# Kernel tuning notes

Hardware: AMD Instinct MI355X
Metric: run time of the kernel (lower is better)

Reference implementation:

```python
import jax, jax.numpy as jnp
import numpy as np

N_NODES = 10000


def _sage_pool(h, src, dst, Wp, bp, Ws, Wn, b):
    # DGL SAGEConv 'pool': m = relu(fc_pool(h_src)); neigh = max over in-edges;
    # out = fc_self(h_dst) + fc_neigh(neigh) + bias. Zero-in-degree nodes get 0 neigh.
    m = jax.nn.relu(h @ Wp + bp)                      # [N, d_in] node-level transform
    neigh = jax.ops.segment_max(m[src], dst, num_segments=N_NODES)  # [N, d_in]
    neigh = jnp.where(jnp.isfinite(neigh), neigh, 0.0)  # empty segments filled -inf -> 0
    return h @ Ws + neigh @ Wn + b


def setup_inputs() -> dict:
    key = jax.random.key(0)
    ks = jax.random.split(key, 20)
    dims = [(960, 512), (512, 512), (512, 1)]
    inp = {
        "h": jax.random.normal(ks[0], (N_NODES, 960), dtype=jnp.float32),
        "src": jax.random.randint(ks[1], (160000,), 0, N_NODES),
        "dst": jax.random.randint(ks[2], (160000,), 0, N_NODES),
    }
    ki = 3
    for l, (di, do) in enumerate(dims):
        inp[f"Wp{l}"] = jax.random.normal(ks[ki + 0], (di, di), dtype=jnp.float32) * 0.02
        inp[f"bp{l}"] = jnp.zeros((di,), dtype=jnp.float32)
        inp[f"Ws{l}"] = jax.random.normal(ks[ki + 1], (di, do), dtype=jnp.float32) * 0.02
        inp[f"Wn{l}"] = jax.random.normal(ks[ki + 2], (di, do), dtype=jnp.float32) * 0.02
        inp[f"b{l}"] = jnp.zeros((do,), dtype=jnp.float32)
        ki += 3
    return inp


def reference(h, src, dst,
              Wp0, bp0, Ws0, Wn0, b0,
              Wp1, bp1, Ws1, Wn1, b1,
              Wp2, bp2, Ws2, Wn2, b2):
    # layer 0: 960 -> 512, relu (dropout = identity in eval)
    x = jax.nn.relu(_sage_pool(h, src, dst, Wp0, bp0, Ws0, Wn0, b0))
    # layer 1: 512 -> 512, relu
    x = jax.nn.relu(_sage_pool(x, src, dst, Wp1, bp1, Ws1, Wn1, b1))
    # layer 2: 512 -> 1, sigmoid, squeeze -> per-node prediction
    x = _sage_pool(x, src, dst, Wp2, bp2, Ws2, Wn2, b2)
    return jax.nn.sigmoid(x).squeeze(-1)  # [N]
```

## Files before the change

### kernel.cpp

```cpp
#include <hip/hip_runtime.h>
#include <stdint.h>

#define NN 10000
#define NE 160000
#define MPAD 10112
#define MTILES 79

typedef unsigned short u16;
typedef float f32x4 __attribute__((ext_vector_type(4)));
typedef short short8 __attribute__((ext_vector_type(8)));
typedef __bf16 bf16x8 __attribute__((ext_vector_type(8)));
typedef unsigned short u16x4 __attribute__((ext_vector_type(4)));
typedef unsigned short u16x8 __attribute__((ext_vector_type(8)));

__device__ __forceinline__ float bf2f(u16 u) {
  union { unsigned u; float f; } c; c.u = ((unsigned)u) << 16; return c.f;
}
__device__ __forceinline__ u16 f2bf(float f) {
  union { float f; unsigned u; } c; c.f = f;
  return (u16)((c.u + 0x7FFFu + ((c.u >> 16) & 1u)) >> 16);
}

__device__ __forceinline__ void gld_lds16(void* lds, const void* g) {
  __builtin_amdgcn_global_load_lds(
      (const unsigned int __attribute__((address_space(1)))*)g,
      (unsigned int __attribute__((address_space(3)))*)lds, 16, 0, 0);
}

__global__ __launch_bounds__(256) void deg_count(const int* __restrict__ dst, int* __restrict__ deg) {
  int e = blockIdx.x * 256 + threadIdx.x;
  if (e < NE) atomicAdd(&deg[dst[e]], 1);
}

__global__ __launch_bounds__(256) void scan_off(const int* __restrict__ deg,
                                                int* __restrict__ roff, int* __restrict__ cur) {
  __shared__ int part[256];
  const int t = threadIdx.x;
  const int CH = 40;
  int s = 0;
  for (int i = 0; i < CH; ++i) { int idx = t * CH + i; if (idx < NN) s += deg[idx]; }
  part[t] = s; __syncthreads();
  for (int off = 1; off < 256; off <<= 1) {
    int v = (t >= off) ? part[t - off] : 0;
    __syncthreads(); part[t] += v; __syncthreads();
  }
  int run = (t == 0) ? 0 : part[t - 1];
  for (int i = 0; i < CH; ++i) {
    int idx = t * CH + i;
    if (idx < NN) { roff[idx] = run; cur[idx] = run; run += deg[idx]; }
  }
  if (t == 255) roff[NN] = NE;
}

__global__ __launch_bounds__(256) void fill_csr(const int* __restrict__ src, const int* __restrict__ dst,
                                                int* __restrict__ cur, int* __restrict__ esrc) {
  int e = blockIdx.x * 256 + threadIdx.x;
  if (e < NE) {
    int p = atomicAdd(&cur[dst[e]], 1);
    esrc[p] = src[e];
  }
}

__global__ __launch_bounds__(256) void convert_h(const float* __restrict__ h, u16* __restrict__ hbf) {
  const size_t i = (size_t)(blockIdx.x * 256 + threadIdx.x) * 4;
  if (i >= (size_t)MPAD * 960) return;
  u16x4 o;
  if (i < (size_t)NN * 960) {
    float4 v = *(const float4*)(h + i);
    o[0] = f2bf(v.x); o[1] = f2bf(v.y); o[2] = f2bf(v.z); o[3] = f2bf(v.w);
  } else {
    o[0] = 0; o[1] = 0; o[2] = 0; o[3] = 0;
  }
  *(u16x4*)(hbf + i) = o;
}

struct WDesc { const float* in; u16* out; int R, C, Cpad, ldo, koff; };
struct WPack { WDesc d[7]; };

__global__ __launch_bounds__(256) void transpose_all(WPack p) {
  const WDesc w = p.d[blockIdx.z];
  const int cb = blockIdx.x * 32, rb = blockIdx.y * 32;
  if (cb >= w.Cpad || rb >= w.R) return;
  __shared__ float tile[32][33];
  const int tx = threadIdx.x & 31, ty = threadIdx.x >> 5;
  for (int i = ty; i < 32; i += 8) {
    int r = rb + i, c = cb + tx;
    tile[i][tx] = (r < w.R && c < w.C) ? w.in[(size_t)r * w.C + c] : 0.f;
  }
  __syncthreads();
  for (int i = ty; i < 32; i += 8) {
    int c = cb + i, r = rb + tx;
    if (c < w.Cpad && r < w.R) w.out[(size_t)c * w.ldo + w.koff + r] = f2bf(tile[tx][i]);
  }
}

template<int TM, int TN, int MINW>
__global__ __launch_bounds__(512, MINW) void gemm3(
    const u16* __restrict__ A0, int lda0,
    const u16* __restrict__ A1, int lda1, int ksplit,
    const u16* __restrict__ B,
    const float* __restrict__ bias, int nbias,
    u16* __restrict__ Cb, int ldcb,
    int K, int act, int tiles_n) {
  constexpr int TR = TM + TN;
  constexpr int NC = TR * 128 / (512 * 16);
  constexpr int WCOLS = 4;
  constexpr int WN = TN / WCOLS;
  constexpr int NJ = WN / 16;
  constexpr int MT = MPAD / TM;
  __shared__ __align__(16) u16 S0[TR * 64];
  __shared__ __align__(16) u16 S1[TR * 64];
  const int tid = threadIdx.x;
  const int wave = tid >> 6, lane = tid & 63;

  const int nwg = tiles_n * MT;
  const int orig = blockIdx.x + blockIdx.y * tiles_n;
  const int q = nwg >> 3, r8 = nwg & 7;
  const int xcd = orig & 7, idx = orig >> 3;
  const int wg = (xcd < r8 ? xcd * (q + 1) : r8 * (q + 1) + (xcd - r8) * q) + idx;
  const int tm = (wg / tiles_n) * TM;
  const int tn = (wg % tiles_n) * TN;

  const int wr = (wave / WCOLS) * 64;
  const int wc = (wave % WCOLS) * WN;
  const int fr = lane & 15, fq = lane >> 4;
  const int sr8 = lane >> 3;
  const int sslot = lane & 7;
  f32x4 acc[4][NJ] = {};

  auto stage = [&](u16* Sw, int kk) {
#pragma unroll
    for (int c = 0; c < NC; ++c) {
      const int row = c * 64 + wave * 8 + sr8;
      const int gs = (sslot ^ (row & 7)) * 8;
      const void* g;
      if (c < NC * TM / TR) {
        g = (kk < ksplit)
            ? (const void*)&A0[(size_t)(tm + row) * lda0 + kk + gs]
            : (const void*)&A1[(size_t)(tm + row) * lda1 + (kk - ksplit) + gs];
      } else {
        g = (const void*)&B[(size_t)(tn + row - TM) * (size_t)K + kk + gs];
      }
      gld_lds16(&Sw[(c * 64 + wave * 8) * 64], g);
    }
  };

  const int nsteps = K >> 6;
  stage(S0, 0);
  stage(S1, 64);
  for (int base = 0; base < nsteps; base += 2) {
#pragma unroll
    for (int ph = 0; ph < 2; ++ph) {
      const int t = base + ph;
      if (t >= nsteps) break;
      u16* Sr = (ph == 0) ? S0 : S1;
      if (t + 1 < nsteps) {
        asm volatile("s_waitcnt vmcnt(%0)" :: "i"(NC) : "memory");
      } else {
        asm volatile("s_waitcnt vmcnt(0)" ::: "memory");
      }
      __builtin_amdgcn_s_barrier();
      __builtin_amdgcn_sched_barrier(0);
      short8 af[4][2], bfr[2][NJ];
#pragma unroll
      for (int i = 0; i < 4; ++i) {
        const int r = wr + i * 16 + fr;
#pragma unroll
        for (int kc = 0; kc < 2; ++kc)
          af[i][kc] = *(const short8*)&Sr[r * 64 + ((((kc << 2) | fq) ^ (r & 7)) << 3)];
      }
#pragma unroll
      for (int j = 0; j < NJ; ++j) {
        const int r = TM + wc + j * 16 + fr;
#pragma unroll
        for (int kc = 0; kc < 2; ++kc)
          bfr[kc][j] = *(const short8*)&Sr[r * 64 + ((((kc << 2) | fq) ^ (r & 7)) << 3)];
      }
      asm volatile("s_waitcnt lgkmcnt(0)" ::: "memory");
      __builtin_amdgcn_sched_barrier(0);
      __builtin_amdgcn_s_barrier();
      if (t + 2 < nsteps) stage(Sr, (t + 2) << 6);
      __builtin_amdgcn_s_setprio(1);
#pragma unroll
      for (int kc = 0; kc < 2; ++kc)
#pragma unroll
        for (int i = 0; i < 4; ++i)
#pragma unroll
          for (int j = 0; j < NJ; ++j)
            acc[i][j] = __builtin_amdgcn_mfma_f32_16x16x32_bf16(
                __builtin_bit_cast(bf16x8, af[i][kc]), __builtin_bit_cast(bf16x8, bfr[kc][j]),
                acc[i][j], 0, 0, 0);
      __builtin_amdgcn_s_setprio(0);
      __builtin_amdgcn_sched_barrier(0);
    }
  }

  const int cr = fq * 4, cc = fr;
#pragma unroll
  for (int i = 0; i < 4; ++i)
#pragma unroll
    for (int j = 0; j < NJ; ++j) {
      const int col = tn + wc + j * 16 + cc;
      const float bv = (col < nbias) ? bias[col] : 0.f;
#pragma unroll
      for (int r = 0; r < 4; ++r) {
        const int row = tm + wr + i * 16 + cr + r;
        float v = acc[i][j][r] + bv;
        if (act) v = fmaxf(v, 0.f);
        Cb[(size_t)row * ldcb + col] = f2bf(v);
      }
    }
}

template<int CW>
__global__ __launch_bounds__(256) void aggregate_xcd(
    const u16* __restrict__ m, int ldm, const int* __restrict__ roff,
    const int* __restrict__ esrc, u16* __restrict__ neigh, int ldn) {
  constexpr int TPN = CW / 8;
  constexpr int NPB = 256 / TPN;
  const int chunk = blockIdx.x & 7;
  const int node = (blockIdx.x >> 3) * NPB + threadIdx.x / TPN;
  if (node >= NN) return;
  const int fi = chunk * CW + (threadIdx.x % TPN) * 8;
  const int beg = roff[node], end = roff[node + 1];
  u16x8 a;
#pragma unroll
  for (int i = 0; i < 8; ++i) a[i] = 0;
  for (int e = beg; e < end; ++e) {
    const u16* row = m + (size_t)esrc[e] * ldm;
    u16x8 v = *(const u16x8*)(row + fi);
#pragma unroll
    for (int i = 0; i < 8; ++i) a[i] = (v[i] > a[i]) ? v[i] : a[i];
  }
  *(u16x8*)(neigh + (size_t)node * ldn + fi) = a;
}

__global__ __launch_bounds__(256) void final_out(
    const u16* __restrict__ x, const u16* __restrict__ neigh,
    const float* __restrict__ ws, const float* __restrict__ wn,
    const float* __restrict__ b, float* __restrict__ out) {
  const int wave = threadIdx.x >> 6, lane = threadIdx.x & 63;
  const int n = blockIdx.x * 4 + wave;
  if (n >= NN) return;
  const int f = lane * 8;
  const u16* xr = x + (size_t)n * 512 + f;
  const u16* nr = neigh + (size_t)n * 512 + f;
  float s = 0.f;
#pragma unroll
  for (int i = 0; i < 8; ++i)
    s += bf2f(xr[i]) * ws[f + i] + bf2f(nr[i]) * wn[f + i];
#pragma unroll
  for (int o = 32; o > 0; o >>= 1) s += __shfl_xor(s, o);
  if (lane == 0) out[n] = 1.f / (1.f + expf(-(s + b[0])));
}

extern "C" void kernel_launch(void* const* d_in, const int* in_sizes, int n_in,
                              void* d_out, int out_size, void* d_ws, size_t ws_size,
                              hipStream_t stream) {
  const float* h   = (const float*)d_in[0];
  const int*   src = (const int*)d_in[1];
  const int*   dst = (const int*)d_in[2];
  const float* Wp0 = (const float*)d_in[3];
  const float* bp0 = (const float*)d_in[4];
  const float* Ws0 = (const float*)d_in[5];
  const float* Wn0 = (const float*)d_in[6];
  const float* b0  = (const float*)d_in[7];
  const float* Wp1 = (const float*)d_in[8];
  const float* bp1 = (const float*)d_in[9];
  const float* Ws1 = (const float*)d_in[10];
  const float* Wn1 = (const float*)d_in[11];
  const float* b1  = (const float*)d_in[12];
  const float* Wp2 = (const float*)d_in[13];
  const float* bp2 = (const float*)d_in[14];
  const float* Ws2 = (const float*)d_in[15];
  const float* Wn2 = (const float*)d_in[16];
  const float* b2  = (const float*)d_in[17];
  float* out = (float*)d_out;

  char* ws = (char*)d_ws;
  size_t off = 0;
  auto alloc = [&](size_t n) { char* p = ws + off; off = (off + n + 255) & ~(size_t)255; return p; };
  u16* hbf   = (u16*)alloc((size_t)MPAD * 960 * 2);
  u16* x1    = (u16*)alloc((size_t)MPAD * 512 * 2);
  u16* x2    = (u16*)alloc((size_t)MPAD * 512 * 2);
  u16* mbuf  = (u16*)alloc((size_t)MPAD * 1024 * 2);
  u16* nbuf  = (u16*)alloc((size_t)MPAD * 1024 * 2);
  u16* WpT0  = (u16*)alloc((size_t)1024 * 960 * 2);
  u16* Bcat0 = (u16*)alloc((size_t)512 * 1920 * 2);
  u16* WpT1  = (u16*)alloc((size_t)512 * 512 * 2);
  u16* Bcat1 = (u16*)alloc((size_t)512 * 1024 * 2);
  u16* WpT2  = (u16*)alloc((size_t)512 * 512 * 2);
  int* deg   = (int*)alloc(NN * 4);
  int* roff  = (int*)alloc((NN + 1) * 4);
  int* curp  = (int*)alloc(NN * 4);
  int* esrc  = (int*)alloc(NE * 4);

  hipMemsetAsync(deg, 0, NN * 4, stream);
  deg_count<<<NE / 256, 256, 0, stream>>>(dst, deg);
  scan_off<<<1, 256, 0, stream>>>(deg, roff, curp);
  fill_csr<<<NE / 256, 256, 0, stream>>>(src, dst, curp, esrc);
  convert_h<<<(MPAD * 960 / 4) / 256, 256, 0, stream>>>(h, hbf);

  WPack wp;
  wp.d[0] = {Wp0, WpT0,  960, 960, 1024,  960,   0};
  wp.d[1] = {Ws0, Bcat0, 960, 512,  512, 1920,   0};
  wp.d[2] = {Wn0, Bcat0, 960, 512,  512, 1920, 960};
  wp.d[3] = {Wp1, WpT1,  512, 512,  512,  512,   0};
  wp.d[4] = {Ws1, Bcat1, 512, 512,  512, 1024,   0};
  wp.d[5] = {Wn1, Bcat1, 512, 512,  512, 1024, 512};
  wp.d[6] = {Wp2, WpT2,  512, 512,  512,  512,   0};
  transpose_all<<<dim3(32, 30, 7), 256, 0, stream>>>(wp);

  gemm3<128, 128, 4><<<dim3(8, 79), 512, 0, stream>>>(
      hbf, 960, hbf, 960, 960, WpT0, bp0, 960, mbuf, 1024, 960, 1, 8);
  aggregate_xcd<128><<<5000, 256, 0, stream>>>(mbuf, 1024, roff, esrc, nbuf, 1024);
  gemm3<128, 128, 4><<<dim3(4, 79), 512, 0, stream>>>(
      hbf, 960, nbuf, 1024, 960, Bcat0, b0, 512, x1, 512, 1920, 1, 4);

  gemm3<128, 128, 4><<<dim3(4, 79), 512, 0, stream>>>(
      x1, 512, x1, 512, 512, WpT1, bp1, 512, mbuf, 512, 512, 1, 4);
  aggregate_xcd<64><<<2504, 256, 0, stream>>>(mbuf, 512, roff, esrc, nbuf, 512);
  gemm3<128, 128, 4><<<dim3(4, 79), 512, 0, stream>>>(
      x1, 512, nbuf, 512, 512, Bcat1, b1, 512, x2, 512, 1024, 1, 4);

  gemm3<128, 128, 4><<<dim3(4, 79), 512, 0, stream>>>(
      x2, 512, x2, 512, 512, WpT2, bp2, 512, mbuf, 512, 512, 1, 4);
  aggregate_xcd<64><<<2504, 256, 0, stream>>>(mbuf, 512, roff, esrc, nbuf, 512);
  final_out<<<2500, 256, 0, stream>>>(x2, nbuf, Ws2, Wn2, b2, out);
}
```

Baseline: 250.9 us.

## Replace direct global-to-LDS loads with register-staged double-buffered GEMM pipeline

```diff
diff --git a/kernel.cpp b/kernel.cpp
--- a/kernel.cpp
+++ b/kernel.cpp
@@ -19,12 +19,6 @@
 __device__ __forceinline__ u16 f2bf(float f) {
   union { float f; unsigned u; } c; c.f = f;
   return (u16)((c.u + 0x7FFFu + ((c.u >> 16) & 1u)) >> 16);
-}
-
-__device__ __forceinline__ void gld_lds16(void* lds, const void* g) {
-  __builtin_amdgcn_global_load_lds(
-      (const unsigned int __attribute__((address_space(1)))*)g,
-      (unsigned int __attribute__((address_space(3)))*)lds, 16, 0, 0);
 }
 
 __global__ __launch_bounds__(256) void deg_count(const int* __restrict__ dst, int* __restrict__ deg) {
@@ -103,7 +97,6 @@
     u16* __restrict__ Cb, int ldcb,
     int K, int act, int tiles_n) {
   constexpr int TR = TM + TN;
-  constexpr int NC = TR * 128 / (512 * 16);
   constexpr int WCOLS = 4;
   constexpr int WN = TN / WCOLS;
   constexpr int NJ = WN / 16;
@@ -128,71 +121,86 @@
   const int sslot = lane & 7;
   f32x4 acc[4][NJ] = {};
 
-  auto stage = [&](u16* Sw, int kk) {
-#pragma unroll
-    for (int c = 0; c < NC; ++c) {
+  const int nsteps = K >> 6;
+
+  auto gloadv = [&](u16x8 (&r)[4], int kk) {
+#pragma unroll
+    for (int c = 0; c < 4; ++c) {
       const int row = c * 64 + wave * 8 + sr8;
-      const int gs = (sslot ^ (row & 7)) * 8;
-      const void* g;
-      if (c < NC * TM / TR) {
-        g = (kk < ksplit)
-            ? (const void*)&A0[(size_t)(tm + row) * lda0 + kk + gs]
-            : (const void*)&A1[(size_t)(tm + row) * lda1 + (kk - ksplit) + gs];
+      if (c < TM / 64) {
+        r[c] = (kk < ksplit)
+            ? *(const u16x8*)&A0[(size_t)(tm + row) * lda0 + kk + sslot * 8]
+            : *(const u16x8*)&A1[(size_t)(tm + row) * lda1 + (kk - ksplit) + sslot * 8];
       } else {
-        g = (const void*)&B[(size_t)(tn + row - TM) * (size_t)K + kk + gs];
+        r[c] = *(const u16x8*)&B[(size_t)(tn + row - TM) * (size_t)K + kk + sslot * 8];
       }
-      gld_lds16(&Sw[(c * 64 + wave * 8) * 64], g);
     }
   };
-
-  const int nsteps = K >> 6;
-  stage(S0, 0);
-  stage(S1, 64);
-  for (int base = 0; base < nsteps; base += 2) {
-#pragma unroll
-    for (int ph = 0; ph < 2; ++ph) {
-      const int t = base + ph;
-      if (t >= nsteps) break;
-      u16* Sr = (ph == 0) ? S0 : S1;
-      if (t + 1 < nsteps) {
-        asm volatile("s_waitcnt vmcnt(%0)" :: "i"(NC) : "memory");
+  auto dswrite = [&](u16* Sw, u16x8 (&r)[4]) {
+#pragma unroll
+    for (int c = 0; c < 4; ++c) {
+      const int row = c * 64 + wave * 8 + sr8;
+      *(u16x8*)&Sw[row * 64 + ((sslot ^ sr8) << 3)] = r[c];
+    }
+  };
+
+  u16x8 rA[4], rB[4];
+  gloadv(rA, 0);
+  asm volatile("s_waitcnt vmcnt(0)" ::: "memory");
+  dswrite(S0, rA);
+  gloadv(rB, 64);
+  asm volatile("s_waitcnt lgkmcnt(0)" ::: "memory");
+
+  auto phase = [&](int t, const u16* Sr, u16* Sw,
+                   u16x8 (&wset)[4], u16x8 (&lset)[4]) {
+    __builtin_amdgcn_s_barrier();
+    __builtin_amdgcn_sched_barrier(0);
+    short8 af[4][2], bfr[2][NJ];
+#pragma unroll
+    for (int i = 0; i < 4; ++i) {
+      const int r = wr + i * 16 + fr;
+#pragma unroll
+      for (int kc = 0; kc < 2; ++kc)
+        af[i][kc] = *(const short8*)&Sr[r * 64 + ((((kc << 2) | fq) ^ (r & 7)) << 3)];
+    }
+#pragma unroll
+    for (int j = 0; j < NJ; ++j) {
+      const int r = TM + wc + j * 16 + fr;
+#pragma unroll
+      for (int kc = 0; kc < 2; ++kc)
+        bfr[kc][j] = *(const short8*)&Sr[r * 64 + ((((kc << 2) | fq) ^ (r & 7)) << 3)];
+    }
+    __builtin_amdgcn_sched_barrier(0);
+    if (t + 2 < nsteps) gloadv(lset, (t + 2) << 6);
+    __builtin_amdgcn_sched_barrier(0);
+    if (t + 1 < nsteps) {
+      if (t + 2 < nsteps) {
+        asm volatile("s_waitcnt vmcnt(4)" ::: "memory");
       } else {
         asm volatile("s_waitcnt vmcnt(0)" ::: "memory");
       }
-      __builtin_amdgcn_s_barrier();
-      __builtin_amdgcn_sched_barrier(0);
-      short8 af[4][2], bfr[2][NJ];
-#pragma unroll
-      for (int i = 0; i < 4; ++i) {
-        const int r = wr + i * 16 + fr;
-#pragma unroll
-        for (int kc = 0; kc < 2; ++kc)
-          af[i][kc] = *(const short8*)&Sr[r * 64 + ((((kc << 2) | fq) ^ (r & 7)) << 3)];
-      }
-#pragma unroll
-      for (int j = 0; j < NJ; ++j) {
-        const int r = TM + wc + j * 16 + fr;
-#pragma unroll
-        for (int kc = 0; kc < 2; ++kc)
-          bfr[kc][j] = *(const short8*)&Sr[r * 64 + ((((kc << 2) | fq) ^ (r & 7)) << 3)];
-      }
-      asm volatile("s_waitcnt lgkmcnt(0)" ::: "memory");
-      __builtin_amdgcn_sched_barrier(0);
-      __builtin_amdgcn_s_barrier();
-      if (t + 2 < nsteps) stage(Sr, (t + 2) << 6);
-      __builtin_amdgcn_s_setprio(1);
-#pragma unroll
-      for (int kc = 0; kc < 2; ++kc)
-#pragma unroll
-        for (int i = 0; i < 4; ++i)
-#pragma unroll
-          for (int j = 0; j < NJ; ++j)
-            acc[i][j] = __builtin_amdgcn_mfma_f32_16x16x32_bf16(
-                __builtin_bit_cast(bf16x8, af[i][kc]), __builtin_bit_cast(bf16x8, bfr[kc][j]),
-                acc[i][j], 0, 0, 0);
-      __builtin_amdgcn_s_setprio(0);
-      __builtin_amdgcn_sched_barrier(0);
-    }
+      dswrite(Sw, wset);
+    }
+    asm volatile("s_waitcnt lgkmcnt(0)" ::: "memory");
+    __builtin_amdgcn_sched_barrier(0);
+    __builtin_amdgcn_s_setprio(1);
+#pragma unroll
+    for (int kc = 0; kc < 2; ++kc)
+#pragma unroll
+      for (int i = 0; i < 4; ++i)
+#pragma unroll
+        for (int j = 0; j < NJ; ++j)
+          acc[i][j] = __builtin_amdgcn_mfma_f32_16x16x32_bf16(
+              __builtin_bit_cast(bf16x8, af[i][kc]), __builtin_bit_cast(bf16x8, bfr[kc][j]),
+              acc[i][j], 0, 0, 0);
+    __builtin_amdgcn_s_setprio(0);
+    __builtin_amdgcn_sched_barrier(0);
+  };
+
+  for (int base = 0; base < nsteps; base += 2) {
+    phase(base, S0, S1, rB, rA);
+    if (base + 1 < nsteps)
+      phase(base + 1, S1, S0, rA, rB);
   }
 
   const int cr = fq * 4, cc = fr;
```

New measurement: 401.1 us. 59.9% more time.

## Stage GEMM tiles through registers instead of direct global-to-LDS loads

Applied to the files above, without the earlier changes.

```diff
diff --git a/kernel.cpp b/kernel.cpp
--- a/kernel.cpp
+++ b/kernel.cpp
@@ -19,12 +19,6 @@
 __device__ __forceinline__ u16 f2bf(float f) {
   union { float f; unsigned u; } c; c.f = f;
   return (u16)((c.u + 0x7FFFu + ((c.u >> 16) & 1u)) >> 16);
-}
-
-__device__ __forceinline__ void gld_lds16(void* lds, const void* g) {
-  __builtin_amdgcn_global_load_lds(
-      (const unsigned int __attribute__((address_space(1)))*)g,
-      (unsigned int __attribute__((address_space(3)))*)lds, 16, 0, 0);
 }
 
 __global__ __launch_bounds__(256) void deg_count(const int* __restrict__ dst, int* __restrict__ deg) {
@@ -94,8 +88,9 @@
   }
 }
 
-template<int TM, int TN, int MINW>
-__global__ __launch_bounds__(512, MINW) void gemm3(
+template<int TM, int TN>
+__global__ __launch_bounds__(512) __attribute__((amdgpu_waves_per_eu(4, 4)))
+void gemm3(
     const u16* __restrict__ A0, int lda0,
     const u16* __restrict__ A1, int lda1, int ksplit,
     const u16* __restrict__ B,
@@ -103,7 +98,6 @@
     u16* __restrict__ Cb, int ldcb,
     int K, int act, int tiles_n) {
   constexpr int TR = TM + TN;
-  constexpr int NC = TR * 128 / (512 * 16);
   constexpr int WCOLS = 4;
   constexpr int WN = TN / WCOLS;
   constexpr int NJ = WN / 16;
@@ -128,72 +122,96 @@
   const int sslot = lane & 7;
   f32x4 acc[4][NJ] = {};
 
-  auto stage = [&](u16* Sw, int kk) {
-#pragma unroll
-    for (int c = 0; c < NC; ++c) {
-      const int row = c * 64 + wave * 8 + sr8;
-      const int gs = (sslot ^ (row & 7)) * 8;
-      const void* g;
-      if (c < NC * TM / TR) {
-        g = (kk < ksplit)
-            ? (const void*)&A0[(size_t)(tm + row) * lda0 + kk + gs]
-            : (const void*)&A1[(size_t)(tm + row) * lda1 + (kk - ksplit) + gs];
-      } else {
-        g = (const void*)&B[(size_t)(tn + row - TM) * (size_t)K + kk + gs];
-      }
-      gld_lds16(&Sw[(c * 64 + wave * 8) * 64], g);
-    }
-  };
-
   const int nsteps = K >> 6;
-  stage(S0, 0);
-  stage(S1, 64);
+
+#define GLOADV(r, kkx)                                                        \
+  {                                                                           \
+    const int kk_ = (kkx);                                                    \
+    _Pragma("unroll")                                                         \
+    for (int c = 0; c < 4; ++c) {                                             \
+      const int row_ = c * 64 + wave * 8 + sr8;                               \
+      if (c < TM / 64) {                                                      \
+        r[c] = (kk_ < ksplit)                                                 \
+            ? *(const u16x8*)&A0[(size_t)(tm + row_) * lda0 + kk_ + sslot * 8]\
+            : *(const u16x8*)&A1[(size_t)(tm + row_) * lda1 + (kk_ - ksplit) + sslot * 8]; \
+      } else {                                                                \
+        r[c] = *(const u16x8*)&B[(size_t)(tn + row_ - TM) * (size_t)K + kk_ + sslot * 8];  \
+      }                                                                       \
+    }                                                                         \
+  }
+
+#define DSWRITE(Sw, r)                                                        \
+  {                                                                           \
+    _Pragma("unroll")                                                         \
+    for (int c = 0; c < 4; ++c) {                                             \
+      const int row_ = c * 64 + wave * 8 + sr8;                               \
+      *(u16x8*)&Sw[row_ * 64 + ((sslot ^ sr8) << 3)] = r[c];                  \
+    }                                                                         \
+  }
+
+#define PHASE(tx, Sr, Sw, wset, lset)                                         \
+  {                                                                           \
+    const int t_ = (tx);                                                      \
+    __builtin_amdgcn_s_barrier();                                             \
+    __builtin_amdgcn_sched_barrier(0);                                        \
+    short8 af[4][2], bfr[2][NJ];                                              \
+    _Pragma("unroll")                                                         \
+    for (int i = 0; i < 4; ++i) {                                             \
+      const int r_ = wr + i * 16 + fr;                                        \
+      _Pragma("unroll")                                                       \
+      for (int kc = 0; kc < 2; ++kc)                                          \
+        af[i][kc] = *(const short8*)&Sr[r_ * 64 + ((((kc << 2) | fq) ^ (r_ & 7)) << 3)]; \
+    }                                                                         \
+    _Pragma("unroll")                                                         \
+    for (int j = 0; j < NJ; ++j) {                                            \
+      const int r_ = TM + wc + j * 16 + fr;                                   \
+      _Pragma("unroll")                                                       \
+      for (int kc = 0; kc < 2; ++kc)                                          \
+        bfr[kc][j] = *(const short8*)&Sr[r_ * 64 + ((((kc << 2) | fq) ^ (r_ & 7)) << 3)]; \
+    }                                                                         \
+    __builtin_amdgcn_sched_barrier(0);                                        \
+    if (t_ + 2 < nsteps) GLOADV(lset, (t_ + 2) << 6);                         \
+    __builtin_amdgcn_sched_barrier(0);                                        \
+    if (t_ + 1 < nsteps) {                                                    \
+      if (t_ + 2 < nsteps) {                                                  \
+        asm volatile("s_waitcnt vmcnt(4)" ::: "memory");                      \
+      } else {                                                                \
+        asm volatile("s_waitcnt vmcnt(0)" ::: "memory");                      \
+      }                                                                       \
+      DSWRITE(Sw, wset);                                                      \
+    }                                                                         \
+    asm volatile("s_waitcnt lgkmcnt(0)" ::: "memory");                        \
+    __builtin_amdgcn_sched_barrier(0);                                        \
+    __builtin_amdgcn_s_setprio(1);                                            \
+    _Pragma("unroll")                                                         \
+    for (int kc = 0; kc < 2; ++kc)                                            \
+      _Pragma("unroll")                                                       \
+      for (int i = 0; i < 4; ++i)                                             \
+        _Pragma("unroll")                                                     \
+        for (int j = 0; j < NJ; ++j)                                          \
+          acc[i][j] = __builtin_amdgcn_mfma_f32_16x16x32_bf16(                \
+              __builtin_bit_cast(bf16x8, af[i][kc]),                          \
+              __builtin_bit_cast(bf16x8, bfr[kc][j]),                         \
+              acc[i][j], 0, 0, 0);                                            \
+    __builtin_amdgcn_s_setprio(0);                                            \
+    __builtin_amdgcn_sched_barrier(0);                                        \
+  }
+
+  u16x8 rA[4], rB[4];
+  GLOADV(rA, 0);
+  asm volatile("s_waitcnt vmcnt(0)" ::: "memory");
+  DSWRITE(S0, rA);
+  GLOADV(rB, 64);
+  asm volatile("s_waitcnt lgkmcnt(0)" ::: "memory");
+
   for (int base = 0; base < nsteps; base += 2) {
-#pragma unroll
-    for (int ph = 0; ph < 2; ++ph) {
-      const int t = base + ph;
-      if (t >= nsteps) break;
-      u16* Sr = (ph == 0) ? S0 : S1;
-      if (t + 1 < nsteps) {
-        asm volatile("s_waitcnt vmcnt(%0)" :: "i"(NC) : "memory");
-      } else {
-        asm volatile("s_waitcnt vmcnt(0)" ::: "memory");
-      }
-      __builtin_amdgcn_s_barrier();
-      __builtin_amdgcn_sched_barrier(0);
-      short8 af[4][2], bfr[2][NJ];
-#pragma unroll
-      for (int i = 0; i < 4; ++i) {
-        const int r = wr + i * 16 + fr;
-#pragma unroll
-        for (int kc = 0; kc < 2; ++kc)
-          af[i][kc] = *(const short8*)&Sr[r * 64 + ((((kc << 2) | fq) ^ (r & 7)) << 3)];
-      }
-#pragma unroll
-      for (int j = 0; j < NJ; ++j) {
-        const int r = TM + wc + j * 16 + fr;
-#pragma unroll
-        for (int kc = 0; kc < 2; ++kc)
-          bfr[kc][j] = *(const short8*)&Sr[r * 64 + ((((kc << 2) | fq) ^ (r & 7)) << 3)];
-      }
-      asm volatile("s_waitcnt lgkmcnt(0)" ::: "memory");
-      __builtin_amdgcn_sched_barrier(0);
-      __builtin_amdgcn_s_barrier();
-      if (t + 2 < nsteps) stage(Sr, (t + 2) << 6);
-      __builtin_amdgcn_s_setprio(1);
-#pragma unroll
-      for (int kc = 0; kc < 2; ++kc)
-#pragma unroll
-        for (int i = 0; i < 4; ++i)
-#pragma unroll
-          for (int j = 0; j < NJ; ++j)
-            acc[i][j] = __builtin_amdgcn_mfma_f32_16x16x32_bf16(
-                __builtin_bit_cast(bf16x8, af[i][kc]), __builtin_bit_cast(bf16x8, bfr[kc][j]),
-                acc[i][j], 0, 0, 0);
-      __builtin_amdgcn_s_setprio(0);
-      __builtin_amdgcn_sched_barrier(0);
-    }
-  }
+    PHASE(base, S0, S1, rB, rA);
+    if (base + 1 < nsteps)
+      PHASE(base + 1, S1, S0, rA, rB);
+  }
+#undef PHASE
+#undef DSWRITE
+#undef GLOADV
 
   const int cr = fq * 4, cc = fr;
 #pragma unroll
@@ -311,19 +329,19 @@
   wp.d[6] = {Wp2, WpT2,  512, 512,  512,  512,   0};
   transpose_all<<<dim3(32, 30, 7), 256, 0, stream>>>(wp);
 
-  gemm3<128, 128, 4><<<dim3(8, 79), 512, 0, stream>>>(
+  gemm3<128, 128><<<dim3(8, 79), 512, 0, stream>>>(
       hbf, 960, hbf, 960, 960, WpT0, bp0, 960, mbuf, 1024, 960, 1, 8);
   aggregate_xcd<128><<<5000, 256, 0, stream>>>(mbuf, 1024, roff, esrc, nbuf, 1024);
-  gemm3<128, 128, 4><<<dim3(4, 79), 512, 0, stream>>>(
+  gemm3<128, 128><<<dim3(4, 79), 512, 0, stream>>>(
       hbf, 960, nbuf, 1024, 960, Bcat0, b0, 512, x1, 512, 1920, 1, 4);
 
-  gemm3<128, 128, 4><<<dim3(4, 79), 512, 0, stream>>>(
+  gemm3<128, 128><<<dim3(4, 79), 512, 0, stream>>>(
       x1, 512, x1, 512, 512, WpT1, bp1, 512, mbuf, 512, 512, 1, 4);
   aggregate_xcd<64><<<2504, 256, 0, stream>>>(mbuf, 512, roff, esrc, nbuf, 512);
-  gemm3<128, 128, 4><<<dim3(4, 79), 512, 0, stream>>>(
+  gemm3<128, 128><<<dim3(4, 79), 512, 0, stream>>>(
       x1, 512, nbuf, 512, 512, Bcat1, b1, 512, x2, 512, 1024, 1, 4);
 
-  gemm3<128, 128, 4><<<dim3(4, 79), 512, 0, stream>>>(
+  gemm3<128, 128><<<dim3(4, 79), 512, 0, stream>>>(
       x2, 512, x2, 512, 512, WpT2, bp2, 512, mbuf, 512, 512, 1, 4);
   aggregate_xcd<64><<<2504, 256, 0, stream>>>(mbuf, 512, roff, esrc, nbuf, 512);
   final_out<<<2500, 256, 0, stream>>>(x2, nbuf, Ws2, Wn2, b2, out);
```

Result: slower. 423.8 us (+68.9%).
